# Kernel tuning notes

Measured on AMD Instinct MI355X. Metric: run time of the kernel, lower is better.

The kernel has to match this reference:

```python
import jax, jax.numpy as jnp
import numpy as np

N_NODES = 50000
N_EDGES = 600000
N_GRAPHS = 256
BN_EPS = 1e-5
NEG_SLOPE = 0.2  # PyG GATv2 default leaky_relu slope


def segment_softmax(logits, seg, num_segments):
    # logits: [E, H], softmax over edges sharing the same destination node
    m = jax.ops.segment_max(logits, seg, num_segments=num_segments)
    e = jnp.exp(logits - m[seg])
    s = jax.ops.segment_sum(e, seg, num_segments=num_segments)
    return e / (s[seg] + 1e-16)


def gatv2_layer(h, edge_attr, src, dst, Wl, bl, Wr, br, We, att, bias, concat):
    # PyG GATv2Conv (share_weights=False, edge_dim set), eval mode (no dropout)
    heads, out_c = att.shape
    N = h.shape[0]
    xl = (h @ Wl + bl).reshape(N, heads, out_c)  # messages from source
    xr = (h @ Wr + br).reshape(N, heads, out_c)  # destination term
    em = (edge_attr @ We).reshape(-1, heads, out_c)
    z = jax.nn.leaky_relu(xl[src] + xr[dst] + em, NEG_SLOPE)  # [E,H,C]
    logits = jnp.einsum('ehc,hc->eh', z, att)
    alpha = segment_softmax(logits, dst, N)  # [E,H]
    out = jax.ops.segment_sum(xl[src] * alpha[:, :, None], dst, num_segments=N)
    out = out.reshape(N, heads * out_c) if concat else out.mean(axis=1)
    return out + bias


def batch_norm(h, gamma, beta):
    mu = h.mean(axis=0)
    var = h.var(axis=0)
    return gamma * (h - mu) * jax.lax.rsqrt(var + BN_EPS) + beta


def setup_inputs() -> dict:
    key = jax.random.key(0)
    ks = jax.random.split(key, 32)
    F, Fe, H, C = 64, 16, 4, 64
    HC = H * C

    def w(k, shape):
        return jax.random.normal(k, shape, dtype=jnp.float32) * 0.1

    inp = {
        'x': jax.random.normal(ks[0], (N_NODES, F), dtype=jnp.float32),
        'edge_attr': jax.random.normal(ks[1], (N_EDGES, Fe), dtype=jnp.float32),
        'edge_index': jax.random.randint(ks[2], (2, N_EDGES), 0, N_NODES, dtype=jnp.int32),
        'batch': jnp.sort(jax.random.randint(ks[3], (N_NODES,), 0, N_GRAPHS, dtype=jnp.int32)),
        # input projection
        'W_in': w(ks[4], (F, C)), 'b_in': jnp.zeros((C,), jnp.float32),
        'Wl0': w(ks[5], (C, HC)), 'bl0': jnp.zeros((HC,), jnp.float32),
        'Wr0': w(ks[6], (C, HC)), 'br0': jnp.zeros((HC,), jnp.float32),
        'We0': w(ks[7], (Fe, HC)),
        'att0': w(ks[8], (H, C)), 'bias0': jnp.zeros((HC,), jnp.float32),
        'g0': jnp.ones((HC,), jnp.float32), 'beta0': jnp.zeros((HC,), jnp.float32),
        'Wl1': w(ks[9], (HC, HC)), 'bl1': jnp.zeros((HC,), jnp.float32),
        'Wr1': w(ks[10], (HC, HC)), 'br1': jnp.zeros((HC,), jnp.float32),
        'We1': w(ks[11], (Fe, HC)),
        'att1': w(ks[12], (H, C)), 'bias1': jnp.zeros((C,), jnp.float32),
        'g1': jnp.ones((C,), jnp.float32), 'beta1': jnp.zeros((C,), jnp.float32),
        # MLP head 64 -> 32 -> 16 -> 1
        'Wm1': w(ks[13], (C, C // 2)), 'bm1': jnp.zeros((C // 2,), jnp.float32),
        'Wm2': w(ks[14], (C // 2, C // 4)), 'bm2': jnp.zeros((C // 4,), jnp.float32),
        'Wm3': w(ks[15], (C // 4, 1)), 'bm3': jnp.zeros((1,), jnp.float32),
    }
    return inp


def reference(x, edge_attr, W_in, b_in,
              Wl0, bl0, Wr0, br0, We0, att0, bias0, g0, beta0,
              Wl1, bl1, Wr1, br1, We1, att1, bias1, g1, beta1,
              Wm1, bm1, Wm2, bm2, Wm3, bm3,
              edge_index, batch):
    src, dst = edge_index[0], edge_index[1]
    h = jax.nn.relu(x @ W_in + b_in)
    h = gatv2_layer(h, edge_attr, src, dst, Wl0, bl0, Wr0, br0, We0, att0, bias0, True)
    h = batch_norm(h, g0, beta0)
    h = jax.nn.relu(h)  # dropout is identity in eval mode
    h = gatv2_layer(h, edge_attr, src, dst, Wl1, bl1, Wr1, br1, We1, att1, bias1, False)
    h = batch_norm(h, g1, beta1)
    # global mean pool over graphs
    cnt = jax.ops.segment_sum(jnp.ones((h.shape[0],), h.dtype), batch, num_segments=N_GRAPHS)
    pooled = jax.ops.segment_sum(h, batch, num_segments=N_GRAPHS) / jnp.maximum(cnt, 1.0)[:, None]
    z = jax.nn.relu(pooled @ Wm1 + bm1)
    z = jax.nn.relu(z @ Wm2 + bm2)
    return z @ Wm3 + bm3  # [N_GRAPHS, 1]
```

## Files before the change

### kernel.cpp

```cpp
#include <hip/hip_runtime.h>
#include <math.h>

constexpr int NN = 50000;
constexpr int NE = 600000;
constexpr int NG = 256;
constexpr int SB = (NN + 255) / 256;
constexpr float kBnEps = 1e-5f;
constexpr float kSlope = 0.2f;

__device__ __forceinline__ float rdlane(float v, int l) {
    return __builtin_bit_cast(float, __builtin_amdgcn_readlane(__builtin_bit_cast(int, v), l));
}

template <int CTRL>
__device__ __forceinline__ float dppadd(float v) {
    int t = __builtin_amdgcn_mov_dpp(__builtin_bit_cast(int, v), CTRL, 0xF, 0xF, true);
    return v + __builtin_bit_cast(float, t);
}
__device__ __forceinline__ float sum16(float v) {
    v = dppadd<0xB1>(v);
    v = dppadd<0x4E>(v);
    v = dppadd<0x141>(v);
    v = dppadd<0x140>(v);
    return v;
}

__device__ __forceinline__ float4 fma4(float a, float4 b, float4 c) {
    c.x = fmaf(a, b.x, c.x); c.y = fmaf(a, b.y, c.y);
    c.z = fmaf(a, b.z, c.z); c.w = fmaf(a, b.w, c.w);
    return c;
}

__global__ __launch_bounds__(256) void k_hist(const int* __restrict__ dst, int* __restrict__ cnt)
{
    int e = blockIdx.x * 256 + threadIdx.x;
    if (e < NE) atomicAdd(&cnt[dst[e]], 1);
}

__global__ __launch_bounds__(256) void k_scanA(const int* __restrict__ cnt,
                                               int* __restrict__ offs, int* __restrict__ bsum)
{
    __shared__ int s[256];
    int tid = threadIdx.x;
    int i = blockIdx.x * 256 + tid;
    int v = (i < NN) ? cnt[i] : 0;
    s[tid] = v;
    __syncthreads();
    #pragma unroll
    for (int d = 1; d < 256; d <<= 1) {
        int u = (tid >= d) ? s[tid - d] : 0;
        __syncthreads();
        s[tid] += u;
        __syncthreads();
    }
    if (i < NN) offs[i] = s[tid];
    if (tid == 255) bsum[blockIdx.x] = s[255];
}

__global__ __launch_bounds__(256) void k_scanB(int* __restrict__ bsum)
{
    __shared__ int s[256];
    int t = threadIdx.x;
    int v = (t < SB) ? bsum[t] : 0;
    s[t] = v;
    __syncthreads();
    #pragma unroll
    for (int d = 1; d < 256; d <<= 1) {
        int u = (t >= d) ? s[t - d] : 0;
        __syncthreads();
        s[t] += u;
        __syncthreads();
    }
    if (t < SB) bsum[t] = s[t];
}

__global__ __launch_bounds__(256) void k_scanC(const int* __restrict__ cnt,
                                               const int* __restrict__ bsum,
                                               int* __restrict__ offs, int* __restrict__ cur)
{
    int i = blockIdx.x * 256 + threadIdx.x;
    if (i > NN) return;
    if (i == NN) { offs[NN] = NE; return; }
    int pre = (blockIdx.x > 0) ? bsum[blockIdx.x - 1] : 0;
    int v = offs[i] - cnt[i] + pre;
    offs[i] = v;
    cur[i] = v;
}

__global__ __launch_bounds__(256) void k_scatter(const int* __restrict__ dst,
                                                 const int* __restrict__ src,
                                                 const float* __restrict__ ea,
                                                 int* __restrict__ cur,
                                                 int* __restrict__ srcs,
                                                 float* __restrict__ eas)
{
    int e = blockIdx.x * 256 + threadIdx.x;
    if (e < NE) {
        int p = atomicAdd(&cur[dst[e]], 1);
        srcs[p] = src[e];
        const float4* s4 = (const float4*)(ea + (size_t)e * 16);
        float4* d4 = (float4*)(eas + (size_t)p * 16);
        d4[0] = s4[0]; d4[1] = s4[1]; d4[2] = s4[2]; d4[3] = s4[3];
    }
}

__global__ __launch_bounds__(256) void k_lin0(
    const float* __restrict__ x, const float* __restrict__ Win,
    const float* __restrict__ bin, const float* __restrict__ WL,
    const float* __restrict__ WR, const float* __restrict__ bl,
    const float* __restrict__ br, float* __restrict__ outl,
    float* __restrict__ outr)
{
    int tid = threadIdx.x;
    int lane = tid & 63, wave = tid >> 6;
    int row0 = blockIdx.x * 32 + wave * 8;

    float xreg[8];
    #pragma unroll
    for (int j = 0; j < 8; ++j) {
        int row = row0 + j; if (row >= NN) row = NN - 1;
        xreg[j] = x[(size_t)row * 64 + lane];
    }
    float h0r[8];
    float b0 = bin[lane];
    #pragma unroll
    for (int j = 0; j < 8; ++j) h0r[j] = b0;
    for (int k = 0; k < 64; ++k) {
        float w = Win[k * 64 + lane];
        #pragma unroll
        for (int j = 0; j < 8; ++j) h0r[j] = fmaf(rdlane(xreg[j], k), w, h0r[j]);
    }
    #pragma unroll
    for (int j = 0; j < 8; ++j) h0r[j] = fmaxf(h0r[j], 0.f);

    float4 accL[8], accR[8];
    #pragma unroll
    for (int j = 0; j < 8; ++j) {
        accL[j] = make_float4(0.f, 0.f, 0.f, 0.f);
        accR[j] = make_float4(0.f, 0.f, 0.f, 0.f);
    }
    for (int k = 0; k < 64; ++k) {
        float4 wl4 = ((const float4*)(WL + (size_t)k * 256))[lane];
        float4 wr4 = ((const float4*)(WR + (size_t)k * 256))[lane];
        #pragma unroll
        for (int j = 0; j < 8; ++j) {
            float hb = rdlane(h0r[j], k);
            accL[j] = fma4(hb, wl4, accL[j]);
            accR[j] = fma4(hb, wr4, accR[j]);
        }
    }
    float4 bl4 = ((const float4*)bl)[lane];
    float4 br4 = ((const float4*)br)[lane];
    #pragma unroll
    for (int j = 0; j < 8; ++j) {
        int row = row0 + j;
        if (row < NN) {
            float4 o;
            o.x = accL[j].x + bl4.x; o.y = accL[j].y + bl4.y;
            o.z = accL[j].z + bl4.z; o.w = accL[j].w + bl4.w;
            ((float4*)(outl + (size_t)row * 256))[lane] = o;
            float4 pp;
            pp.x = accR[j].x + br4.x; pp.y = accR[j].y + br4.y;
            pp.z = accR[j].z + br4.z; pp.w = accR[j].w + br4.w;
            ((float4*)(outr + (size_t)row * 256))[lane] = pp;
        }
    }
}

template <int K, bool BN>
__global__ __launch_bounds__(256) void k_linear2(
    const float* __restrict__ h, const float* __restrict__ WL,
    const float* __restrict__ WR, const float* __restrict__ bl,
    const float* __restrict__ br, const float* __restrict__ scale,
    const float* __restrict__ shift, float* __restrict__ outl,
    float* __restrict__ outr)
{
    int tid = threadIdx.x;
    int lane = tid & 63, wave = tid >> 6;
    int row0 = blockIdx.x * 32 + wave * 8;
    int q = lane >> 4;
    int kl = lane & 15;
    float4 accL[8], accR[8];
    #pragma unroll
    for (int r = 0; r < 8; ++r) {
        accL[r] = make_float4(0.f, 0.f, 0.f, 0.f);
        accR[r] = make_float4(0.f, 0.f, 0.f, 0.f);
    }

    for (int kt = 0; kt < K / 16; ++kt) {
        float hreg[2];
        float sc = 1.f, sh = 0.f;
        if (BN) { sc = scale[kt * 16 + kl]; sh = shift[kt * 16 + kl]; }
        #pragma unroll
        for (int r = 0; r < 2; ++r) {
            int row = row0 + 4 * r + q;
            if (row >= NN) row = NN - 1;
            float v = h[(size_t)row * K + kt * 16 + kl];
            if (BN) v = fmaxf(fmaf(v, sc, sh), 0.f);
            hreg[r] = v;
        }
        #pragma unroll
        for (int k = 0; k < 16; ++k) {
            float4 wl4 = ((const float4*)(WL + (size_t)(kt * 16 + k) * 256))[lane];
            float4 wr4 = ((const float4*)(WR + (size_t)(kt * 16 + k) * 256))[lane];
            #pragma unroll
            for (int j = 0; j < 8; ++j) {
                float hb = rdlane(hreg[j >> 2], (j & 3) * 16 + k);
                accL[j] = fma4(hb, wl4, accL[j]);
                accR[j] = fma4(hb, wr4, accR[j]);
            }
        }
    }
    float4 bl4 = ((const float4*)bl)[lane];
    float4 br4 = ((const float4*)br)[lane];
    #pragma unroll
    for (int j = 0; j < 8; ++j) {
        int row = row0 + j;
        if (row < NN) {
            float4 o;
            o.x = accL[j].x + bl4.x; o.y = accL[j].y + bl4.y;
            o.z = accL[j].z + bl4.z; o.w = accL[j].w + bl4.w;
            ((float4*)(outl + (size_t)row * 256))[lane] = o;
            float4 pp;
            pp.x = accR[j].x + br4.x; pp.y = accR[j].y + br4.y;
            pp.z = accR[j].z + br4.z; pp.w = accR[j].w + br4.w;
            ((float4*)(outr + (size_t)row * 256))[lane] = pp;
        }
    }
}

template <bool CONCAT, int NPW>
__global__ __launch_bounds__(256) void k_attn(
    const float* __restrict__ xl, const float* __restrict__ xr,
    const float* __restrict__ eas, const float* __restrict__ We,
    const float* __restrict__ att, const int* __restrict__ srcs,
    const int* __restrict__ offs, const float* __restrict__ bias,
    float* __restrict__ out)
{
    int tid = threadIdx.x;
    int lane = tid & 63, wave = tid >> 6;
    float4 wr[16];
    #pragma unroll
    for (int k = 0; k < 16; ++k) wr[k] = ((const float4*)(We + k * 256))[lane];
    float4 ar = ((const float4*)att)[lane];

    int g16 = lane >> 4;
    int k16 = lane & 15;
    int nodebase = (blockIdx.x * 4 + wave) * NPW;
    if (nodebase >= NN) return;

    for (int nn = 0; nn < NPW; ++nn) {
        int n = nodebase + nn;
        if (n >= NN) break;
        int beg = offs[n], end = offs[n + 1];
        float4 xr4 = ((const float4*)(xr + (size_t)n * 256))[lane];

        float m = -INFINITY, ssum = 0.f;
        float4 acc = make_float4(0.f, 0.f, 0.f, 0.f);

        float nea = 0.f;
        float4 nx0, nx1, nx2, nx3;

        auto loadbatch = [&](int i) {
            int idx = i + g16;
            if (idx > end - 1) idx = end - 1;
            nea = eas[(size_t)idx * 16 + k16];
            int sv = srcs[idx];
            int s0 = __builtin_amdgcn_readlane(sv, 0);
            int s1 = __builtin_amdgcn_readlane(sv, 16);
            int s2 = __builtin_amdgcn_readlane(sv, 32);
            int s3 = __builtin_amdgcn_readlane(sv, 48);
            nx0 = ((const float4*)(xl + (size_t)s0 * 256))[lane];
            nx1 = ((const float4*)(xl + (size_t)s1 * 256))[lane];
            nx2 = ((const float4*)(xl + (size_t)s2 * 256))[lane];
            nx3 = ((const float4*)(xl + (size_t)s3 * 256))[lane];
        };

        if (beg < end) loadbatch(beg);

        for (int i = beg; i < end; i += 4) {
            float cea = nea;
            float4 x0 = nx0, x1 = nx1, x2 = nx2, x3 = nx3;
            if (i + 4 < end) loadbatch(i + 4);

            float p[4];
            #pragma unroll
            for (int g = 0; g < 4; ++g) {
                float4 xg = (g == 0) ? x0 : (g == 1) ? x1 : (g == 2) ? x2 : x3;
                float4 em = xr4;
                #pragma unroll
                for (int k = 0; k < 16; ++k) {
                    float a = rdlane(cea, g * 16 + k);
                    em.x = fmaf(a, wr[k].x, em.x);
                    em.y = fmaf(a, wr[k].y, em.y);
                    em.z = fmaf(a, wr[k].z, em.z);
                    em.w = fmaf(a, wr[k].w, em.w);
                }
                float z0 = xg.x + em.x;
                float z1 = xg.y + em.y;
                float z2 = xg.z + em.z;
                float z3 = xg.w + em.w;
                z0 = (z0 > 0.f) ? z0 : kSlope * z0;
                z1 = (z1 > 0.f) ? z1 : kSlope * z1;
                z2 = (z2 > 0.f) ? z2 : kSlope * z2;
                z3 = (z3 > 0.f) ? z3 : kSlope * z3;
                float pv = fmaf(z0, ar.x, fmaf(z1, ar.y, fmaf(z2, ar.z, z3 * ar.w)));
                pv = sum16(pv);
                p[g] = (i + g < end) ? pv : -INFINITY;
            }
            float pm = fmaxf(fmaxf(p[0], p[1]), fmaxf(p[2], p[3]));
            float mn = fmaxf(m, pm);
            float sc = __expf(m - mn);
            float w0 = __expf(p[0] - mn);
            float w1 = __expf(p[1] - mn);
            float w2 = __expf(p[2] - mn);
            float w3 = __expf(p[3] - mn);
            ssum = fmaf(ssum, sc, (w0 + w1) + (w2 + w3));
            acc.x = fmaf(acc.x, sc, fmaf(w0, x0.x, fmaf(w1, x1.x, fmaf(w2, x2.x, w3 * x3.x))));
            acc.y = fmaf(acc.y, sc, fmaf(w0, x0.y, fmaf(w1, x1.y, fmaf(w2, x2.y, w3 * x3.y))));
            acc.z = fmaf(acc.z, sc, fmaf(w0, x0.z, fmaf(w1, x1.z, fmaf(w2, x2.z, w3 * x3.z))));
            acc.w = fmaf(acc.w, sc, fmaf(w0, x0.w, fmaf(w1, x1.w, fmaf(w2, x2.w, w3 * x3.w))));
            m = mn;
        }

        float inv = 1.f / (ssum + 1e-16f);
        if (CONCAT) {
            float4 b4 = ((const float4*)bias)[lane];
            float4 o;
            o.x = fmaf(acc.x, inv, b4.x);
            o.y = fmaf(acc.y, inv, b4.y);
            o.z = fmaf(acc.z, inv, b4.z);
            o.w = fmaf(acc.w, inv, b4.w);
            ((float4*)(out + (size_t)n * 256))[lane] = o;
        } else {
            float v0 = acc.x * inv, v1 = acc.y * inv, v2 = acc.z * inv, v3 = acc.w * inv;
            v0 += __shfl_xor(v0, 16, 64); v0 += __shfl_xor(v0, 32, 64);
            v1 += __shfl_xor(v1, 16, 64); v1 += __shfl_xor(v1, 32, 64);
            v2 += __shfl_xor(v2, 16, 64); v2 += __shfl_xor(v2, 32, 64);
            v3 += __shfl_xor(v3, 16, 64); v3 += __shfl_xor(v3, 32, 64);
            if (lane < 16) {
                float4 b4 = ((const float4*)bias)[lane];
                float4 o;
                o.x = fmaf(0.25f, v0, b4.x);
                o.y = fmaf(0.25f, v1, b4.y);
                o.z = fmaf(0.25f, v2, b4.z);
                o.w = fmaf(0.25f, v3, b4.w);
                ((float4*)(out + (size_t)n * 64))[lane] = o;
            }
        }
    }
}

template <int CH>
__global__ __launch_bounds__(256) void k_bn_stats(const float* __restrict__ h,
                                                  float* __restrict__ sum,
                                                  float* __restrict__ sumsq)
{
    constexpr int RP = 256 / CH;
    int tid = threadIdx.x;
    int c = tid % CH;
    int rsub = tid / CH;
    float s = 0.f, q = 0.f;
    for (int n = blockIdx.x * RP + rsub; n < NN; n += gridDim.x * RP) {
        float v = h[(size_t)n * CH + c];
        s += v; q = fmaf(v, v, q);
    }
    __shared__ float ls[256], lq[256];
    ls[tid] = s; lq[tid] = q;
    __syncthreads();
    if (tid < CH) {
        #pragma unroll
        for (int r = 1; r < RP; ++r) { s += ls[tid + r * CH]; q += lq[tid + r * CH]; }
        atomicAdd(&sum[tid], s);
        atomicAdd(&sumsq[tid], q);
    }
}

__global__ void k_bn_finalize(const float* __restrict__ sum, const float* __restrict__ sumsq,
                              const float* __restrict__ g, const float* __restrict__ beta,
                              float* __restrict__ scale, float* __restrict__ shift, int CH)
{
    int c = threadIdx.x;
    if (c >= CH) return;
    float inv_n = 1.f / (float)NN;
    float mu = sum[c] * inv_n;
    float var = sumsq[c] * inv_n - mu * mu;
    float sc = g[c] / sqrtf(var + kBnEps);
    scale[c] = sc;
    shift[c] = fmaf(-mu, sc, beta[c]);
}

__global__ __launch_bounds__(256) void k_pool_mlp(
    const float* __restrict__ h2, const float* __restrict__ scale,
    const float* __restrict__ shift, const int* __restrict__ batch,
    const float* __restrict__ Wm1, const float* __restrict__ bm1,
    const float* __restrict__ Wm2, const float* __restrict__ bm2,
    const float* __restrict__ Wm3, const float* __restrict__ bm3,
    float* __restrict__ out)
{
    int g = blockIdx.x, tid = threadIdx.x;
    int lane = tid & 63, wave = tid >> 6;
    __shared__ int sb[2];
    if (tid < 2) {
        int target = g + tid;
        int lo = 0, hi = NN;
        while (lo < hi) {
            int mid = (lo + hi) >> 1;
            if (batch[mid] < target) lo = mid + 1; else hi = mid;
        }
        sb[tid] = lo;
    }
    __syncthreads();
    int s = sb[0], e = sb[1];
    float sc = scale[lane], sh = shift[lane];
    float acc = 0.f;
    for (int n = s + wave; n < e; n += 4)
        acc += fmaf(h2[(size_t)n * 64 + lane], sc, sh);
    __shared__ float red[4][64];
    red[wave][lane] = acc;
    __syncthreads();
    __shared__ float p[64], z1[32], z2[16];
    if (tid < 64) {
        float cnt = (float)(e - s);
        float a = red[0][tid] + red[1][tid] + red[2][tid] + red[3][tid];
        p[tid] = a / fmaxf(cnt, 1.f);
    }
    __syncthreads();
    if (tid < 32) {
        float a = bm1[tid];
        #pragma unroll
        for (int k = 0; k < 64; ++k) a = fmaf(p[k], Wm1[k * 32 + tid], a);
        z1[tid] = fmaxf(a, 0.f);
    }
    __syncthreads();
    if (tid < 16) {
        float a = bm2[tid];
        #pragma unroll
        for (int k = 0; k < 32; ++k) a = fmaf(z1[k], Wm2[k * 16 + tid], a);
        z2[tid] = fmaxf(a, 0.f);
    }
    __syncthreads();
    if (tid == 0) {
        float a = bm3[0];
        #pragma unroll
        for (int k = 0; k < 16; ++k) a = fmaf(z2[k], Wm3[k], a);
        out[g] = a;
    }
}

extern "C" void kernel_launch(void* const* d_in, const int* in_sizes, int n_in,
                              void* d_out, int out_size, void* d_ws, size_t ws_size,
                              hipStream_t stream)
{
    const float* x     = (const float*)d_in[0];
    const float* ea    = (const float*)d_in[1];
    const int*   ei    = (const int*)d_in[2];
    const int*   bat   = (const int*)d_in[3];
    const float* W_in  = (const float*)d_in[4];
    const float* b_in  = (const float*)d_in[5];
    const float* Wl0   = (const float*)d_in[6];
    const float* bl0   = (const float*)d_in[7];
    const float* Wr0   = (const float*)d_in[8];
    const float* br0   = (const float*)d_in[9];
    const float* We0   = (const float*)d_in[10];
    const float* att0  = (const float*)d_in[11];
    const float* bias0 = (const float*)d_in[12];
    const float* g0    = (const float*)d_in[13];
    const float* beta0 = (const float*)d_in[14];
    const float* Wl1   = (const float*)d_in[15];
    const float* bl1   = (const float*)d_in[16];
    const float* Wr1   = (const float*)d_in[17];
    const float* br1   = (const float*)d_in[18];
    const float* We1   = (const float*)d_in[19];
    const float* att1  = (const float*)d_in[20];
    const float* bias1 = (const float*)d_in[21];
    const float* g1    = (const float*)d_in[22];
    const float* beta1 = (const float*)d_in[23];
    const float* Wm1   = (const float*)d_in[24];
    const float* bm1   = (const float*)d_in[25];
    const float* Wm2   = (const float*)d_in[26];
    const float* bm2   = (const float*)d_in[27];
    const float* Wm3   = (const float*)d_in[28];
    const float* bm3   = (const float*)d_in[29];
    const int* src = ei;
    const int* dst = ei + NE;
    float* out = (float*)d_out;

    char* p = (char*)d_ws;
    auto take = [&](size_t nbytes) -> char* {
        char* q = p;
        p += (nbytes + 255) & ~(size_t)255;
        return q;
    };
    char* z0 = p;
    int*   hist   = (int*)take((size_t)NN * 4);
    float* bns0   = (float*)take(256 * 4);
    float* bnq0   = (float*)take(256 * 4);
    float* bns1   = (float*)take(64 * 4);
    float* bnq1   = (float*)take(64 * 4);
    size_t zbytes = (size_t)(p - z0);
    int*   offs   = (int*)take((size_t)(NN + 1) * 4);
    int*   curs   = (int*)take((size_t)NN * 4);
    int*   bsum   = (int*)take((size_t)SB * 4);
    int*   srcs   = (int*)take((size_t)NE * 4);
    float* eas    = (float*)take((size_t)NE * 16 * 4);
    float* h2     = (float*)take((size_t)NN * 64 * 4);
    float* xl     = (float*)take((size_t)NN * 256 * 4);
    float* xr     = (float*)take((size_t)NN * 256 * 4);
    float* h1     = (float*)take((size_t)NN * 256 * 4);
    float* scale0 = (float*)take(256 * 4);
    float* shift0 = (float*)take(256 * 4);
    float* scale1 = (float*)take(64 * 4);
    float* shift1 = (float*)take(64 * 4);

    hipMemsetAsync(z0, 0, zbytes, stream);

    k_hist<<<(NE + 255) / 256, 256, 0, stream>>>(dst, hist);
    k_scanA<<<SB, 256, 0, stream>>>(hist, offs, bsum);
    k_scanB<<<1, 256, 0, stream>>>(bsum);
    k_scanC<<<SB, 256, 0, stream>>>(hist, bsum, offs, curs);
    k_scatter<<<(NE + 255) / 256, 256, 0, stream>>>(dst, src, ea, curs, srcs, eas);

    constexpr int NPW = 2;
    int attn_blocks = (NN + 4 * NPW - 1) / (4 * NPW);
    int lin_blocks = (NN + 31) / 32;

    k_lin0<<<lin_blocks, 256, 0, stream>>>(
        x, W_in, b_in, Wl0, Wr0, bl0, br0, xl, xr);
    k_attn<true, NPW><<<attn_blocks, 256, 0, stream>>>(
        xl, xr, eas, We0, att0, srcs, offs, bias0, h1);
    k_bn_stats<256><<<256, 256, 0, stream>>>(h1, bns0, bnq0);
    k_bn_finalize<<<1, 256, 0, stream>>>(bns0, bnq0, g0, beta0, scale0, shift0, 256);

    k_linear2<256, true><<<lin_blocks, 256, 0, stream>>>(
        h1, Wl1, Wr1, bl1, br1, scale0, shift0, xl, xr);
    k_attn<false, NPW><<<attn_blocks, 256, 0, stream>>>(
        xl, xr, eas, We1, att1, srcs, offs, bias1, h2);
    k_bn_stats<64><<<256, 256, 0, stream>>>(h2, bns1, bnq1);
    k_bn_finalize<<<1, 64, 0, stream>>>(bns1, bnq1, g1, beta1, scale1, shift1, 64);

    k_pool_mlp<<<NG, 256, 0, stream>>>(h2, scale1, shift1, bat,
                                       Wm1, bm1, Wm2, bm2, Wm3, bm3, out);
}
```

Measured before the change: 808.3 us.

## Run layer-1 projection on MFMA with split-fp16 hi/lo emulation of fp32

Replaces the scalar-FMA layer-1 linear kernel (256->512 outputs, fused BN+ReLU on input) with an MFMA 32x32x16 fp16 kernel. Both activations and weights are split into fp16 hi and lo parts, and three MFMAs per tile approximate fp32 accuracy. A new prep kernel packs the weights into an MFMA-friendly layout, and the activations are staged through swizzled LDS. The goal is to cut compute time of the largest dense matmul, at the cost of an extra launch, 3x MFMA work, and a small precision risk from dropping the lo*lo term and fp16 range limits.

```diff
diff --git a/kernel.cpp b/kernel.cpp
--- a/kernel.cpp
+++ b/kernel.cpp
@@ -7,6 +7,9 @@
 constexpr int SB = (NN + 255) / 256;
 constexpr float kBnEps = 1e-5f;
 constexpr float kSlope = 0.2f;
+
+typedef _Float16 f16x8 __attribute__((ext_vector_type(8)));
+typedef float f32x16 __attribute__((ext_vector_type(16)));
 
 __device__ __forceinline__ float rdlane(float v, int l) {
     return __builtin_bit_cast(float, __builtin_amdgcn_readlane(__builtin_bit_cast(int, v), l));
@@ -163,6 +166,119 @@
             pp.x = accR[j].x + br4.x; pp.y = accR[j].y + br4.y;
             pp.z = accR[j].z + br4.z; pp.w = accR[j].w + br4.w;
             ((float4*)(outr + (size_t)row * 256))[lane] = pp;
+        }
+    }
+}
+
+__global__ __launch_bounds__(256) void k_prep_w(const float* __restrict__ WL,
+                                                const float* __restrict__ WR,
+                                                _Float16* __restrict__ bhi,
+                                                _Float16* __restrict__ blo)
+{
+    int T = blockIdx.x * 256 + threadIdx.x;
+    int g   = T & 1;
+    int col = (T >> 1) & 511;
+    int kt  = T >> 10;
+    const float* W = (col < 256) ? WL : WR;
+    int c = col & 255;
+    f16x8 h8, l8;
+    #pragma unroll
+    for (int i = 0; i < 8; ++i) {
+        float v = W[(size_t)(kt * 16 + g * 8 + i) * 256 + c];
+        _Float16 hv = (_Float16)v;
+        h8[i] = hv;
+        l8[i] = (_Float16)(v - (float)hv);
+    }
+    *(f16x8*)(bhi + (size_t)T * 8) = h8;
+    *(f16x8*)(blo + (size_t)T * 8) = l8;
+}
+
+__global__ __launch_bounds__(256) void k_linear2_mfma(
+    const float* __restrict__ h, const _Float16* __restrict__ Bhi,
+    const _Float16* __restrict__ Blo, const float* __restrict__ bl,
+    const float* __restrict__ br, const float* __restrict__ scale,
+    const float* __restrict__ shift, float* __restrict__ outl,
+    float* __restrict__ outr)
+{
+    __shared__ f16x8 Apack[2][16][64];
+    int tid = threadIdx.x;
+    int lane = tid & 63, wave = tid >> 6;
+    int row0 = blockIdx.x * 32;
+
+    {
+        int row  = tid >> 3;
+        int koff = (tid & 7) * 32;
+        int grow = row0 + row; if (grow >= NN) grow = NN - 1;
+        const float* hp = h + (size_t)grow * 256 + koff;
+        #pragma unroll
+        for (int j2 = 0; j2 < 4; ++j2) {
+            int o = koff + j2 * 8;
+            float4 a  = *(const float4*)(hp + j2 * 8);
+            float4 b  = *(const float4*)(hp + j2 * 8 + 4);
+            float4 s0 = *(const float4*)(scale + o);
+            float4 s1 = *(const float4*)(scale + o + 4);
+            float4 f0 = *(const float4*)(shift + o);
+            float4 f1 = *(const float4*)(shift + o + 4);
+            float va[8] = {
+                fmaxf(fmaf(a.x, s0.x, f0.x), 0.f), fmaxf(fmaf(a.y, s0.y, f0.y), 0.f),
+                fmaxf(fmaf(a.z, s0.z, f0.z), 0.f), fmaxf(fmaf(a.w, s0.w, f0.w), 0.f),
+                fmaxf(fmaf(b.x, s1.x, f1.x), 0.f), fmaxf(fmaf(b.y, s1.y, f1.y), 0.f),
+                fmaxf(fmaf(b.z, s1.z, f1.z), 0.f), fmaxf(fmaf(b.w, s1.w, f1.w), 0.f)};
+            f16x8 hi8, lo8;
+            #pragma unroll
+            for (int i = 0; i < 8; ++i) {
+                _Float16 hv = (_Float16)va[i];
+                hi8[i] = hv;
+                lo8[i] = (_Float16)(va[i] - (float)hv);
+            }
+            int kt = o >> 4, g = (o >> 3) & 1;
+            int slot = (g * 32 + row) ^ (kt & 7);
+            Apack[0][kt][slot] = hi8;
+            Apack[1][kt][slot] = lo8;
+        }
+    }
+    __syncthreads();
+
+    int g = lane >> 5;
+    int colbase = wave * 128 + (lane & 31);
+    f32x16 acc[4];
+    #pragma unroll
+    for (int nt = 0; nt < 4; ++nt)
+        #pragma unroll
+        for (int r = 0; r < 16; ++r) acc[nt][r] = 0.f;
+
+    const f16x8* bh = (const f16x8*)Bhi;
+    const f16x8* bo = (const f16x8*)Blo;
+    size_t fbase = (size_t)colbase * 2 + g;
+
+    #pragma unroll 4
+    for (int kt = 0; kt < 16; ++kt) {
+        f16x8 ahi = Apack[0][kt][lane ^ (kt & 7)];
+        f16x8 alo = Apack[1][kt][lane ^ (kt & 7)];
+        #pragma unroll
+        for (int nt = 0; nt < 4; ++nt) {
+            size_t fi = fbase + (size_t)kt * 1024 + nt * 64;
+            f16x8 wh = bh[fi];
+            f16x8 wl = bo[fi];
+            acc[nt] = __builtin_amdgcn_mfma_f32_32x32x16_f16(ahi, wh, acc[nt], 0, 0, 0);
+            acc[nt] = __builtin_amdgcn_mfma_f32_32x32x16_f16(alo, wh, acc[nt], 0, 0, 0);
+            acc[nt] = __builtin_amdgcn_mfma_f32_32x32x16_f16(ahi, wl, acc[nt], 0, 0, 0);
+        }
+    }
+
+    #pragma unroll
+    for (int nt = 0; nt < 4; ++nt) {
+        int col = colbase + nt * 32;
+        bool isR = col >= 256;
+        int c = isR ? col - 256 : col;
+        float bv = isR ? br[c] : bl[c];
+        float* outp = isR ? outr : outl;
+        #pragma unroll
+        for (int r = 0; r < 16; ++r) {
+            int rowoff = (r & 3) + 8 * (r >> 2) + 4 * g;
+            int grow = row0 + rowoff;
+            if (grow < NN)
+                outp[(size_t)grow * 256 + c] = acc[nt][r] + bv;
         }
     }
 }
@@ -512,10 +628,13 @@
     float* shift0 = (float*)take(256 * 4);
     float* scale1 = (float*)take(64 * 4);
     float* shift1 = (float*)take(64 * 4);
+    _Float16* Bhi1 = (_Float16*)take((size_t)256 * 512 * 2);
+    _Float16* Blo1 = (_Float16*)take((size_t)256 * 512 * 2);
 
     hipMemsetAsync(z0, 0, zbytes, stream);
 
     k_hist<<<(NE + 255) / 256, 256, 0, stream>>>(dst, hist);
+    k_prep_w<<<64, 256, 0, stream>>>(Wl1, Wr1, Bhi1, Blo1);
     k_scanA<<<SB, 256, 0, stream>>>(hist, offs, bsum);
     k_scanB<<<1, 256, 0, stream>>>(bsum);
     k_scanC<<<SB, 256, 0, stream>>>(hist, bsum, offs, curs);
@@ -532,8 +651,8 @@
     k_bn_stats<256><<<256, 256, 0, stream>>>(h1, bns0, bnq0);
     k_bn_finalize<<<1, 256, 0, stream>>>(bns0, bnq0, g0, beta0, scale0, shift0, 256);
 
-    k_linear2<256, true><<<lin_blocks, 256, 0, stream>>>(
-        h1, Wl1, Wr1, bl1, br1, scale0, shift0, xl, xr);
+    k_linear2_mfma<<<lin_blocks, 256, 0, stream>>>(
+        h1, Bhi1, Blo1, bl1, br1, scale0, shift0, xl, xr);
     k_attn<false, NPW><<<attn_blocks, 256, 0, stream>>>(
         xl, xr, eas, We1, att1, srcs, offs, bias1, h2);
     k_bn_stats<64><<<256, 256, 0, stream>>>(h2, bns1, bnq1);
```

After: 751.6 us. 7.0% less time.
